# Kernel tuning notes

Measured on AMD Instinct MI355X. Metric: run time of the kernel, lower is better.

## Reference

```python
import jax, jax.numpy as jnp
import numpy as np

N, E, FEAT, EMB, HID, V, EA, G = 10000, 250000, 16, 32, 32, 12, 9, 64
TEMP = 1.0


def setup_inputs() -> dict:
    key = jax.random.key(0)
    ks = jax.random.split(key, 20)
    p = lambda k, shp: jax.random.normal(k, shp, dtype=jnp.float32) * 0.05
    return {
        "x": jax.random.normal(ks[0], (N, FEAT), dtype=jnp.float32),
        "edge_attr": jax.random.normal(ks[1], (E, EA), dtype=jnp.float32),
        "edge_index": jax.random.randint(ks[2], (2, E), 0, N),
        "batch": jnp.sort(jax.random.randint(ks[3], (N,), 0, G)),
        # conv1 edge MLP: Linear(EA,32) -> ReLU -> Linear(32, FEAT*EMB)
        "nn1_w1": p(ks[4], (EA, 32)), "nn1_b1": p(ks[5], (32,)),
        "nn1_w2": p(ks[6], (32, FEAT * EMB)), "nn1_b2": p(ks[7], (FEAT * EMB,)),
        "root1": p(ks[8], (FEAT, EMB)), "bias1": p(ks[9], (EMB,)),
        # conv2 edge MLP: Linear(EA,32) -> ReLU -> Linear(32, EMB*HID)
        "nn2_w1": p(ks[10], (EA, 32)), "nn2_b1": p(ks[11], (32,)),
        "nn2_w2": p(ks[12], (32, EMB * HID)), "nn2_b2": p(ks[13], (EMB * HID,)),
        "root2": p(ks[14], (EMB, HID)), "bias2": p(ks[15], (HID,)),
        "lin_w": p(ks[16], (HID, V)), "lin_b": p(ks[17], (V,)),
    }


def _segment_mean(vals, ids, num_segments):
    s = jax.ops.segment_sum(vals, ids, num_segments=num_segments)
    cnt = jax.ops.segment_sum(jnp.ones((vals.shape[0],), vals.dtype), ids,
                              num_segments=num_segments)
    return s / jnp.maximum(cnt, 1.0)[:, None]


def _nnconv(h, edge_attr, src, dst, w1, b1, w2, b2, root, bias, din, dout):
    # edge MLP -> per-edge weight matrix [E, din, dout]
    we = (jax.nn.relu(edge_attr @ w1 + b1) @ w2 + b2).reshape(-1, din, dout)
    msg = jnp.einsum('ei,eio->eo', h[src], we)      # gather + per-edge matmul
    agg = _segment_mean(msg, dst, h.shape[0])       # scatter-mean to targets
    return agg + h @ root + bias                    # root weight + bias


def reference(x, edge_attr, edge_index, batch,
              nn1_w1, nn1_b1, nn1_w2, nn1_b2, root1, bias1,
              nn2_w1, nn2_b1, nn2_w2, nn2_b2, root2, bias2,
              lin_w, lin_b):
    src, dst = edge_index[0], edge_index[1]
    h = jax.nn.relu(_nnconv(x, edge_attr, src, dst,
                            nn1_w1, nn1_b1, nn1_w2, nn1_b2, root1, bias1,
                            FEAT, EMB))
    h = jax.nn.relu(_nnconv(h, edge_attr, src, dst,
                            nn2_w1, nn2_b1, nn2_w2, nn2_b2, root2, bias2,
                            EMB, HID))
    pooled = _segment_mean(h, batch, G)             # global_mean_pool [G, HID]
    logits = (pooled @ lin_w + lin_b) / TEMP
    return jax.nn.log_softmax(logits, axis=1)
```

## Files before the change

kernel.cpp:

```cpp
#include <hip/hip_runtime.h>
#include <hip/hip_bf16.h>
#include <stdint.h>

#define NN 10000
#define NE 250000
#define FEAT 16
#define EMB 32
#define HID 32
#define NV 12
#define EAD 9
#define NG 64
#define NCH 25

__device__ __forceinline__ uint32_t bf16rne(float f) {
    uint32_t u = __float_as_uint(f);
    return (u + 0x7fffu + ((u >> 16) & 1u)) >> 16;
}
__device__ __forceinline__ float blo(uint32_t p) { return __uint_as_float(p << 16); }
__device__ __forceinline__ float bhi(uint32_t p) { return __uint_as_float(p & 0xffff0000u); }

__global__ void edge_stats_kernel(const int* __restrict__ dst,
                                  int* __restrict__ histD) {
    int e = blockIdx.x * blockDim.x + threadIdx.x;
    if (e >= NE) return;
    atomicAdd(&histD[dst[e]], 1);
}

__global__ __launch_bounds__(1024) void scan_kernel(const int* __restrict__ hist,
                                                    int* __restrict__ rowStart,
                                                    int* __restrict__ cursor) {
    __shared__ int part[1024];
    int t = threadIdx.x;
    int base = t * 10;
    int local[10];
    int s = 0;
#pragma unroll
    for (int i = 0; i < 10; ++i) {
        int v = (base + i < NN) ? hist[base + i] : 0;
        local[i] = s;
        s += v;
    }
    part[t] = s;
    __syncthreads();
    for (int off = 1; off < 1024; off <<= 1) {
        int v = (t >= off) ? part[t - off] : 0;
        __syncthreads();
        part[t] += v;
        __syncthreads();
    }
    int pre = (t == 0) ? 0 : part[t - 1];
#pragma unroll
    for (int i = 0; i < 10; ++i) {
        if (base + i < NN) {
            int rs = pre + local[i];
            rowStart[base + i] = rs;
            cursor[base + i] = rs;
        }
    }
    if (t == 1023) rowStart[NN] = part[1023];
}

__global__ void scatter_kernel(const float* __restrict__ ea,
                               const int* __restrict__ src,
                               const int* __restrict__ dst,
                               int* __restrict__ cursorD,
                               float* __restrict__ ea_d,
                               int* __restrict__ src_d) {
    int e = blockIdx.x * blockDim.x + threadIdx.x;
    if (e >= NE) return;
    int dv = dst[e];
    int pos = atomicAdd(&cursorD[dv], 1);
    src_d[pos] = src[e];
#pragma unroll
    for (int j = 0; j < 12; ++j)
        ea_d[(size_t)pos * 12 + j] = (j < EAD) ? ea[(size_t)e * EAD + j] : 0.f;
}

template <int DIN>
__global__ __launch_bounds__(256) void computeQ_pack_kernel(
    const float* __restrict__ h,
    const float* __restrict__ w2,
    uint32_t* __restrict__ Qp)
{
    int t = threadIdx.x;
    int o = t & 31;
    int kk = (blockIdx.y * 256 + t) >> 5;
    float w0[DIN], w1r[DIN];
    const float* wa = w2 + (size_t)(2 * kk) * (DIN * 32) + o;
    const float* wb = w2 + (size_t)(2 * kk + 1) * (DIN * 32) + o;
#pragma unroll
    for (int i = 0; i < DIN; ++i) { w0[i] = wa[i * 32]; w1r[i] = wb[i * 32]; }

    int n0 = blockIdx.x * NCH;
    for (int j = 0; j < NCH; ++j) {
        int n = n0 + j;
        const float* hn = h + (size_t)n * DIN;
        float s0 = 0.f, s1 = 0.f;
#pragma unroll
        for (int i = 0; i < DIN; ++i) {
            float hv = hn[i];
            s0 += hv * w0[i];
            s1 += hv * w1r[i];
        }
        Qp[((size_t)n * 16 + kk) * 32 + o] = (bf16rne(s1) << 16) | bf16rne(s0);
    }
}

template <int DIN>
__global__ void computeQbias_kernel(const float* __restrict__ h,
                                    const float* __restrict__ b2,
                                    float* __restrict__ Qb) {
    int idx = blockIdx.x * blockDim.x + threadIdx.x;
    if (idx >= NN * 32) return;
    int o = idx & 31;
    int n = idx >> 5;
    const float* hn = h + (size_t)n * DIN;
    float s = 0.f;
#pragma unroll
    for (int i = 0; i < DIN; ++i) s += hn[i] * b2[i * 32 + o];
    Qb[idx] = s;
}

template <int DIN, bool POOL>
__global__ __launch_bounds__(256) void conv_fused_kernel(
    const float* __restrict__ ea_d,
    const int* __restrict__ src_d,
    const int* __restrict__ rowD,
    const float* __restrict__ w1,
    const float* __restrict__ b1,
    const uint32_t* __restrict__ Qp,
    const float* __restrict__ Qb,
    const float* __restrict__ hin,
    const float* __restrict__ root,
    const float* __restrict__ bias,
    float* __restrict__ hout,
    float* __restrict__ pooled,
    const int* __restrict__ batch,
    float* __restrict__ gcnt)
{
    __shared__ float s_hid[4][2][32];
    int t = threadIdx.x;
    int wv = t >> 6;
    int lane = t & 63;
    int half = lane >> 5;
    int o = lane & 31;

    float w1r[EAD];
#pragma unroll
    for (int j = 0; j < EAD; ++j) w1r[j] = w1[j * 32 + o];
    float b1r = b1[o];

    int n = blockIdx.x * 4 + wv;
    int beg = rowD[n], end = rowD[n + 1];

    float acc = 0.f;
    for (int e = beg + half; e < end; e += 2) {
        const float4* eav = (const float4*)(ea_d + (size_t)e * 12);
        float4 a0 = eav[0], a1 = eav[1], a2 = eav[2];
        float hs = b1r;
        hs += a0.x * w1r[0] + a0.y * w1r[1] + a0.z * w1r[2] + a0.w * w1r[3];
        hs += a1.x * w1r[4] + a1.y * w1r[5] + a1.z * w1r[6] + a1.w * w1r[7];
        hs += a2.x * w1r[8];
        float hd = fmaxf(hs, 0.f);

        s_hid[wv][half][o] = hd;
        __builtin_amdgcn_wave_barrier();

        int sv = src_d[e];
        const uint32_t* q = Qp + (size_t)sv * 512 + o;
        float m = Qb[(size_t)sv * 32 + o];
        const float4* hq = (const float4*)(&s_hid[wv][half][0]);
#pragma unroll
        for (int c = 0; c < 8; ++c) {
            float4 hv = hq[c];
            uint32_t qa  = q[(2 * c) * 32];
            uint32_t qb2 = q[(2 * c + 1) * 32];
            m += hv.x * blo(qa) + hv.y * bhi(qa)
               + hv.z * blo(qb2) + hv.w * bhi(qb2);
        }
        acc += m;
        __builtin_amdgcn_wave_barrier();
    }

    acc += __shfl_xor(acc, 32);

    float inv = 1.0f / fmaxf((float)(end - beg), 1.0f);
    float s = acc * inv + bias[o];
    const float* hrow = hin + (size_t)n * DIN;
#pragma unroll
    for (int i = 0; i < DIN; ++i) s += hrow[i] * root[i * 32 + o];
    s = fmaxf(s, 0.f);

    if (half == 0) {
        hout[(size_t)n * 32 + o] = s;
        if (POOL) {
            int g = batch[n];
            atomicAdd(&pooled[g * 32 + o], s);
            if (o == 0) atomicAdd(&gcnt[g], 1.0f);
        }
    }
}

__global__ void final_kernel(const float* __restrict__ pooled,
                             const float* __restrict__ gcnt,
                             const float* __restrict__ lin_w,
                             const float* __restrict__ lin_b,
                             float* __restrict__ out) {
    int g = threadIdx.x;
    if (g >= NG) return;
    float inv = 1.0f / fmaxf(gcnt[g], 1.0f);
    float p[HID];
#pragma unroll
    for (int h = 0; h < HID; ++h) p[h] = pooled[g * HID + h] * inv;
    float logits[NV];
    float mx = -1e30f;
#pragma unroll
    for (int v = 0; v < NV; ++v) {
        float s = lin_b[v];
#pragma unroll
        for (int h = 0; h < HID; ++h) s += p[h] * lin_w[h * NV + v];
        logits[v] = s;
        mx = fmaxf(mx, s);
    }
    float se = 0.f;
#pragma unroll
    for (int v = 0; v < NV; ++v) se += expf(logits[v] - mx);
    float lse = mx + logf(se);
#pragma unroll
    for (int v = 0; v < NV; ++v) out[g * NV + v] = logits[v] - lse;
}

extern "C" void kernel_launch(void* const* d_in, const int* in_sizes, int n_in,
                              void* d_out, int out_size, void* d_ws, size_t ws_size,
                              hipStream_t stream) {
    const float* x        = (const float*)d_in[0];
    const float* ea       = (const float*)d_in[1];
    const int*   eidx     = (const int*)d_in[2];
    const int*   batch    = (const int*)d_in[3];
    const float* nn1_w1   = (const float*)d_in[4];
    const float* nn1_b1   = (const float*)d_in[5];
    const float* nn1_w2   = (const float*)d_in[6];
    const float* nn1_b2   = (const float*)d_in[7];
    const float* root1    = (const float*)d_in[8];
    const float* bias1    = (const float*)d_in[9];
    const float* nn2_w1   = (const float*)d_in[10];
    const float* nn2_b1   = (const float*)d_in[11];
    const float* nn2_w2   = (const float*)d_in[12];
    const float* nn2_b2   = (const float*)d_in[13];
    const float* root2    = (const float*)d_in[14];
    const float* bias2    = (const float*)d_in[15];
    const float* lin_w    = (const float*)d_in[16];
    const float* lin_b    = (const float*)d_in[17];
    float* out = (float*)d_out;

    const int* src = eidx;
    const int* dst = eidx + NE;

    char* base = (char*)d_ws;
    uint32_t* Qp   = (uint32_t*)base;
    float* ea_d    = (float*)(Qp + (size_t)NN * 512);
    float* Qb      = ea_d + (size_t)NE * 12;
    float* h1      = Qb + (size_t)NN * 32;
    float* h2      = h1 + (size_t)NN * 32;
    int*   src_d   = (int*)(h2 + (size_t)NN * 32);
    int*   rowD    = src_d + NE;
    int*   curD    = rowD + NN + 1;
    int*   histD   = curD + NN;
    float* pooled  = (float*)(histD + NN);
    float* gcnt    = pooled + NG * 32;
    size_t zero_bytes = ((size_t)NN + NG * 32 + NG) * 4;

    hipMemsetAsync(histD, 0, zero_bytes, stream);

    edge_stats_kernel<<<(NE + 255) / 256, 256, 0, stream>>>(dst, histD);
    scan_kernel<<<1, 1024, 0, stream>>>(histD, rowD, curD);
    scatter_kernel<<<(NE + 255) / 256, 256, 0, stream>>>(ea, src, dst, curD,
                                                         ea_d, src_d);

    dim3 qgrid(NN / NCH, 2);
    const int conv_grid = NN / 4;

    computeQ_pack_kernel<FEAT><<<qgrid, 256, 0, stream>>>(x, nn1_w2, Qp);
    computeQbias_kernel<FEAT><<<(NN * 32) / 256, 256, 0, stream>>>(x, nn1_b2, Qb);
    conv_fused_kernel<FEAT, false><<<conv_grid, 256, 0, stream>>>(
        ea_d, src_d, rowD, nn1_w1, nn1_b1, Qp, Qb,
        x, root1, bias1, h1, nullptr, nullptr, nullptr);

    computeQ_pack_kernel<EMB><<<qgrid, 256, 0, stream>>>(h1, nn2_w2, Qp);
    computeQbias_kernel<EMB><<<(NN * 32) / 256, 256, 0, stream>>>(h1, nn2_b2, Qb);
    conv_fused_kernel<EMB, true><<<conv_grid, 256, 0, stream>>>(
        ea_d, src_d, rowD, nn2_w1, nn2_b1, Qp, Qb,
        h1, root2, bias2, h2, pooled, batch, gcnt);

    final_kernel<<<1, 64, 0, stream>>>(pooled, gcnt, lin_w, lin_b, out);
}
```

Measured before the change: 289.4 us.

## Reassociate NNConv into per-node outer-product accumulation followed by dense GEMM

Replaces the per-source precomputed bf16 Q tables with a different factorisation. For each target node, a new kernel accumulates the sum over incoming edges of the outer product of the hidden edge-MLP activation and the source features, plus the plain sum of the source features. A tiled dense GEMM against w2/b2 then produces the messages. This removes the large per-node Q table writes and the per-edge gathers of 512 words. It also drops the bf16 quantisation, so the maths stays in fp32. In exchange it writes and reads an intermediate of 33*DIN floats per node and runs a scalar shared-memory GEMM.

```diff
diff --git a/kernel.cpp b/kernel.cpp
--- a/kernel.cpp
+++ b/kernel.cpp
@@ -10,14 +10,6 @@
 #define NV 12
 #define EAD 9
 #define NG 64
-#define NCH 25
-
-__device__ __forceinline__ uint32_t bf16rne(float f) {
-    uint32_t u = __float_as_uint(f);
-    return (u + 0x7fffu + ((u >> 16) & 1u)) >> 16;
-}
-__device__ __forceinline__ float blo(uint32_t p) { return __uint_as_float(p << 16); }
-__device__ __forceinline__ float bhi(uint32_t p) { return __uint_as_float(p & 0xffff0000u); }
 
 __global__ void edge_stats_kernel(const int* __restrict__ dst,
                                   int* __restrict__ histD) {
@@ -77,59 +69,74 @@
 }
 
 template <int DIN>
-__global__ __launch_bounds__(256) void computeQ_pack_kernel(
-    const float* __restrict__ h,
-    const float* __restrict__ w2,
-    uint32_t* __restrict__ Qp)
-{
-    int t = threadIdx.x;
-    int o = t & 31;
-    int kk = (blockIdx.y * 256 + t) >> 5;
-    float w0[DIN], w1r[DIN];
-    const float* wa = w2 + (size_t)(2 * kk) * (DIN * 32) + o;
-    const float* wb = w2 + (size_t)(2 * kk + 1) * (DIN * 32) + o;
-#pragma unroll
-    for (int i = 0; i < DIN; ++i) { w0[i] = wa[i * 32]; w1r[i] = wb[i * 32]; }
-
-    int n0 = blockIdx.x * NCH;
-    for (int j = 0; j < NCH; ++j) {
-        int n = n0 + j;
-        const float* hn = h + (size_t)n * DIN;
-        float s0 = 0.f, s1 = 0.f;
-#pragma unroll
-        for (int i = 0; i < DIN; ++i) {
-            float hv = hn[i];
-            s0 += hv * w0[i];
-            s1 += hv * w1r[i];
-        }
-        Qp[((size_t)n * 16 + kk) * 32 + o] = (bf16rne(s1) << 16) | bf16rne(s0);
-    }
-}
-
-template <int DIN>
-__global__ void computeQbias_kernel(const float* __restrict__ h,
-                                    const float* __restrict__ b2,
-                                    float* __restrict__ Qb) {
-    int idx = blockIdx.x * blockDim.x + threadIdx.x;
-    if (idx >= NN * 32) return;
-    int o = idx & 31;
-    int n = idx >> 5;
-    const float* hn = h + (size_t)n * DIN;
-    float s = 0.f;
-#pragma unroll
-    for (int i = 0; i < DIN; ++i) s += hn[i] * b2[i * 32 + o];
-    Qb[idx] = s;
-}
-
-template <int DIN, bool POOL>
-__global__ __launch_bounds__(256) void conv_fused_kernel(
+__global__ __launch_bounds__(256) void cbuild_kernel(
     const float* __restrict__ ea_d,
     const int* __restrict__ src_d,
     const int* __restrict__ rowD,
     const float* __restrict__ w1,
     const float* __restrict__ b1,
-    const uint32_t* __restrict__ Qp,
-    const float* __restrict__ Qb,
+    const float* __restrict__ h,
+    float* __restrict__ C)
+{
+    constexpr int IB = DIN / 2;
+    constexpr int K = 33 * DIN;
+    int t = threadIdx.x;
+    int l = t & 63;
+    int n = blockIdx.x * 4 + (t >> 6);
+    int k = l & 31;
+    int ih = l >> 5;
+
+    float w1r[EAD];
+#pragma unroll
+    for (int j = 0; j < EAD; ++j) w1r[j] = w1[j * 32 + k];
+    float b1r = b1[k];
+
+    float c[IB], sb[IB];
+#pragma unroll
+    for (int j = 0; j < IB; ++j) { c[j] = 0.f; sb[j] = 0.f; }
+
+    int beg = rowD[n], end = rowD[n + 1];
+    for (int e = beg; e < end; ++e) {
+        const float4* eav = (const float4*)(ea_d + (size_t)e * 12);
+        float4 a0 = eav[0], a1 = eav[1], a2 = eav[2];
+        float hs = b1r;
+        hs += a0.x * w1r[0] + a0.y * w1r[1] + a0.z * w1r[2] + a0.w * w1r[3];
+        hs += a1.x * w1r[4] + a1.y * w1r[5] + a1.z * w1r[6] + a1.w * w1r[7];
+        hs += a2.x * w1r[8];
+        float hd = fmaxf(hs, 0.f);
+
+        int sv = src_d[e];
+        const float* hr = h + (size_t)sv * DIN + ih * IB;
+#pragma unroll
+        for (int j4 = 0; j4 < IB / 4; ++j4) {
+            float4 hv = *(const float4*)(hr + j4 * 4);
+            c[j4 * 4 + 0] += hd * hv.x;  sb[j4 * 4 + 0] += hv.x;
+            c[j4 * 4 + 1] += hd * hv.y;  sb[j4 * 4 + 1] += hv.y;
+            c[j4 * 4 + 2] += hd * hv.z;  sb[j4 * 4 + 2] += hv.z;
+            c[j4 * 4 + 3] += hd * hv.w;  sb[j4 * 4 + 3] += hv.w;
+        }
+    }
+
+    float* cb = C + (size_t)n * K + k * DIN + ih * IB;
+#pragma unroll
+    for (int j4 = 0; j4 < IB / 4; ++j4)
+        *(float4*)(cb + j4 * 4) =
+            make_float4(c[j4 * 4], c[j4 * 4 + 1], c[j4 * 4 + 2], c[j4 * 4 + 3]);
+    if (k == 0) {
+        float* sbp = C + (size_t)n * K + 32 * DIN + ih * IB;
+#pragma unroll
+        for (int j4 = 0; j4 < IB / 4; ++j4)
+            *(float4*)(sbp + j4 * 4) =
+                make_float4(sb[j4 * 4], sb[j4 * 4 + 1], sb[j4 * 4 + 2], sb[j4 * 4 + 3]);
+    }
+}
+
+template <int DIN, bool POOL>
+__global__ __launch_bounds__(256) void gemm_node_kernel(
+    const float* __restrict__ C,
+    const float* __restrict__ w2,
+    const float* __restrict__ b2,
+    const int* __restrict__ rowD,
     const float* __restrict__ hin,
     const float* __restrict__ root,
     const float* __restrict__ bias,
@@ -138,64 +145,73 @@
     const int* __restrict__ batch,
     float* __restrict__ gcnt)
 {
-    __shared__ float s_hid[4][2][32];
+    constexpr int K = 33 * DIN;
+    constexpr int KT = 132;
+    constexpr int NT = K / KT;
+    __shared__ float sW[KT * 32];
+    __shared__ float sC[32 * KT];
+    __shared__ float sroot[DIN * 32];
+    __shared__ float sh[32 * DIN];
+    __shared__ int sdeg[32];
+
     int t = threadIdx.x;
-    int wv = t >> 6;
-    int lane = t & 63;
-    int half = lane >> 5;
-    int o = lane & 31;
-
-    float w1r[EAD];
-#pragma unroll
-    for (int j = 0; j < EAD; ++j) w1r[j] = w1[j * 32 + o];
-    float b1r = b1[o];
-
-    int n = blockIdx.x * 4 + wv;
-    int beg = rowD[n], end = rowD[n + 1];
-
-    float acc = 0.f;
-    for (int e = beg + half; e < end; e += 2) {
-        const float4* eav = (const float4*)(ea_d + (size_t)e * 12);
-        float4 a0 = eav[0], a1 = eav[1], a2 = eav[2];
-        float hs = b1r;
-        hs += a0.x * w1r[0] + a0.y * w1r[1] + a0.z * w1r[2] + a0.w * w1r[3];
-        hs += a1.x * w1r[4] + a1.y * w1r[5] + a1.z * w1r[6] + a1.w * w1r[7];
-        hs += a2.x * w1r[8];
-        float hd = fmaxf(hs, 0.f);
-
-        s_hid[wv][half][o] = hd;
-        __builtin_amdgcn_wave_barrier();
-
-        int sv = src_d[e];
-        const uint32_t* q = Qp + (size_t)sv * 512 + o;
-        float m = Qb[(size_t)sv * 32 + o];
-        const float4* hq = (const float4*)(&s_hid[wv][half][0]);
-#pragma unroll
-        for (int c = 0; c < 8; ++c) {
-            float4 hv = hq[c];
-            uint32_t qa  = q[(2 * c) * 32];
-            uint32_t qb2 = q[(2 * c + 1) * 32];
-            m += hv.x * blo(qa) + hv.y * bhi(qa)
-               + hv.z * blo(qb2) + hv.w * bhi(qb2);
-        }
-        acc += m;
-        __builtin_amdgcn_wave_barrier();
-    }
-
-    acc += __shfl_xor(acc, 32);
-
-    float inv = 1.0f / fmaxf((float)(end - beg), 1.0f);
-    float s = acc * inv + bias[o];
-    const float* hrow = hin + (size_t)n * DIN;
-#pragma unroll
-    for (int i = 0; i < DIN; ++i) s += hrow[i] * root[i * 32 + o];
-    s = fmaxf(s, 0.f);
-
-    if (half == 0) {
-        hout[(size_t)n * 32 + o] = s;
+    int o = t & 31;
+    int ng = t >> 5;
+    int n0 = blockIdx.x * 32;
+
+    float msum[4] = {0.f, 0.f, 0.f, 0.f};
+
+    for (int kt = 0; kt < NT; ++kt) {
+        __syncthreads();
+        for (int idx = t; idx < KT * 32; idx += 256) {
+            int kk = idx >> 5, o2 = idx & 31;
+            int f = kt * KT + kk;
+            int k = f / DIN, i = f & (DIN - 1);
+            sW[idx] = (k < 32) ? w2[(size_t)k * (DIN * 32) + i * 32 + o2]
+                               : b2[i * 32 + o2];
+        }
+        for (int idx = t; idx < 32 * KT; idx += 256) {
+            int nl = idx / KT, kk = idx - nl * KT;
+            int n = n0 + nl;
+            sC[idx] = (n < NN) ? C[(size_t)n * K + kt * KT + kk] : 0.f;
+        }
+        __syncthreads();
+#pragma unroll 4
+        for (int kk = 0; kk < KT; ++kk) {
+            float w = sW[kk * 32 + o];
+#pragma unroll
+            for (int q = 0; q < 4; ++q)
+                msum[q] += sC[(ng * 4 + q) * KT + kk] * w;
+        }
+    }
+
+    __syncthreads();
+    for (int idx = t; idx < DIN * 32; idx += 256) sroot[idx] = root[idx];
+    for (int idx = t; idx < 32 * DIN; idx += 256) {
+        int nl = idx / DIN, i = idx - nl * DIN;
+        int n = n0 + nl;
+        sh[idx] = (n < NN) ? hin[(size_t)n * DIN + i] : 0.f;
+    }
+    if (t < 32) {
+        int n = n0 + t;
+        sdeg[t] = (n < NN) ? (rowD[n + 1] - rowD[n]) : 1;
+    }
+    __syncthreads();
+
+    float bo = bias[o];
+#pragma unroll
+    for (int q = 0; q < 4; ++q) {
+        int nl = ng * 4 + q;
+        int n = n0 + nl;
+        if (n >= NN) continue;
+        float v = msum[q] / fmaxf((float)sdeg[nl], 1.f) + bo;
+#pragma unroll
+        for (int i = 0; i < DIN; ++i) v += sh[nl * DIN + i] * sroot[i * 32 + o];
+        v = fmaxf(v, 0.f);
+        hout[(size_t)n * 32 + o] = v;
         if (POOL) {
             int g = batch[n];
-            atomicAdd(&pooled[g * 32 + o], s);
+            atomicAdd(&pooled[g * 32 + o], v);
             if (o == 0) atomicAdd(&gcnt[g], 1.0f);
         }
     }
@@ -257,17 +273,16 @@
     const int* dst = eidx + NE;
 
     char* base = (char*)d_ws;
-    uint32_t* Qp   = (uint32_t*)base;
-    float* ea_d    = (float*)(Qp + (size_t)NN * 512);
-    float* Qb      = ea_d + (size_t)NE * 12;
-    float* h1      = Qb + (size_t)NN * 32;
-    float* h2      = h1 + (size_t)NN * 32;
-    int*   src_d   = (int*)(h2 + (size_t)NN * 32);
-    int*   rowD    = src_d + NE;
-    int*   curD    = rowD + NN + 1;
-    int*   histD   = curD + NN;
-    float* pooled  = (float*)(histD + NN);
-    float* gcnt    = pooled + NG * 32;
+    float* Cbuf   = (float*)base;
+    float* ea_d   = Cbuf + (size_t)NN * 1056;
+    float* h1     = ea_d + (size_t)NE * 12;
+    float* h2     = h1 + (size_t)NN * 32;
+    int*   src_d  = (int*)(h2 + (size_t)NN * 32);
+    int*   rowD   = src_d + NE;
+    int*   curD   = rowD + NN + 1;
+    int*   histD  = curD + NN;
+    float* pooled = (float*)(histD + NN);
+    float* gcnt   = pooled + NG * 32;
     size_t zero_bytes = ((size_t)NN + NG * 32 + NG) * 4;
 
     hipMemsetAsync(histD, 0, zero_bytes, stream);
@@ -277,20 +292,20 @@
     scatter_kernel<<<(NE + 255) / 256, 256, 0, stream>>>(ea, src, dst, curD,
                                                          ea_d, src_d);
 
-    dim3 qgrid(NN / NCH, 2);
-    const int conv_grid = NN / 4;
-
-    computeQ_pack_kernel<FEAT><<<qgrid, 256, 0, stream>>>(x, nn1_w2, Qp);
-    computeQbias_kernel<FEAT><<<(NN * 32) / 256, 256, 0, stream>>>(x, nn1_b2, Qb);
-    conv_fused_kernel<FEAT, false><<<conv_grid, 256, 0, stream>>>(
-        ea_d, src_d, rowD, nn1_w1, nn1_b1, Qp, Qb,
-        x, root1, bias1, h1, nullptr, nullptr, nullptr);
-
-    computeQ_pack_kernel<EMB><<<qgrid, 256, 0, stream>>>(h1, nn2_w2, Qp);
-    computeQbias_kernel<EMB><<<(NN * 32) / 256, 256, 0, stream>>>(h1, nn2_b2, Qb);
-    conv_fused_kernel<EMB, true><<<conv_grid, 256, 0, stream>>>(
-        ea_d, src_d, rowD, nn2_w1, nn2_b1, Qp, Qb,
-        h1, root2, bias2, h2, pooled, batch, gcnt);
+    const int cb_grid = NN / 4;
+    const int gn_grid = (NN + 31) / 32;
+
+    cbuild_kernel<FEAT><<<cb_grid, 256, 0, stream>>>(
+        ea_d, src_d, rowD, nn1_w1, nn1_b1, x, Cbuf);
+    gemm_node_kernel<FEAT, false><<<gn_grid, 256, 0, stream>>>(
+        Cbuf, nn1_w2, nn1_b2, rowD, x, root1, bias1, h1,
+        nullptr, nullptr, nullptr);
+
+    cbuild_kernel<EMB><<<cb_grid, 256, 0, stream>>>(
+        ea_d, src_d, rowD, nn2_w1, nn2_b1, h1, Cbuf);
+    gemm_node_kernel<EMB, true><<<gn_grid, 256, 0, stream>>>(
+        Cbuf, nn2_w2, nn2_b2, rowD, h1, root2, bias2, h2,
+        pooled, batch, gcnt);
 
     final_kernel<<<1, 64, 0, stream>>>(pooled, gcnt, lin_w, lin_b, out);
 }
```

Measured after the change: 361.3 us. 24.8% more time.
